# Optimization experiments

Measured on AMD Instinct MI355X. Metric: run time of the kernel, lower is better.

The kernel has to match this reference:

```python
import jax, jax.numpy as jnp
import numpy as np

N, R, M = 2048, 8, 4096  # samples, rank, signal length (M even)


def setup_inputs() -> dict:
    key = jax.random.key(0)
    kW, kH, kT = jax.random.split(key, 3)
    W = jax.random.normal(kW, (N, R), dtype=jnp.float32)
    H = jax.random.normal(kH, (R, M), dtype=jnp.float32)
    # tau are per-(sample, component) time shifts; modest positive values
    tau = jax.random.uniform(kT, (N, R), dtype=jnp.float32) * 5.0
    return {"W": W, "H": H, "tau": tau}


def reference(W, H, tau):
    # W: (N, R) raw weights, H: (R, M) raw sources, tau: (N, R) shifts
    M_ = H.shape[1]
    Nf = M_ // 2 + 1
    # one-sided spectrum of the (softplus-constrained) sources
    Hf = jnp.fft.fft(jax.nn.softplus(H), axis=1)[:, :Nf]            # (R, Nf) complex
    # rebuild full mirrored spectrum: [Hf, conj(flip(Hf[:, 1:Nf-1]))] -> (R, M)
    Hft = jnp.concatenate([Hf, jnp.conj(Hf[:, 1:Nf - 1][:, ::-1])], axis=1)
    f = jnp.arange(M_, dtype=H.dtype) / M_                          # (M,) normalized freqs
    # complex exponential shift operator, (N, R, M)
    omega = jnp.exp(-2j * jnp.pi * jnp.einsum('nd,m->ndm', tau, f))
    Wf = jax.nn.softplus(W)[:, :, None] * omega                     # (N, R, M)
    # reduce over rank: V[n, m] = sum_d Wf[n, d, m] * Hft[d, m]
    V = jnp.einsum('ndm,dm->nm', Wf, Hft)                           # (N, M) complex
    return V
```

## Files before the change

kernel.cpp:

```cpp
#include <hip/hip_runtime.h>
#include <math.h>

#define MLEN 4096
#define RANK 8
#define NSAMP 2048
#define VEC 4
#define NS  4

__device__ __forceinline__ float softplus_f(float x) {
    return (x > 20.0f) ? x : log1pf(expf(x));
}

__global__ __launch_bounds__(1024) void fft_rows_kernel(const float* __restrict__ H,
                                                        float2* __restrict__ Hft) {
    __shared__ float2 buf[MLEN];
    const int d = blockIdx.x;
    const float* row = H + d * MLEN;

    for (int i = threadIdx.x; i < MLEN; i += 1024) {
        unsigned x = __brev((unsigned)i) >> 20;
        unsigned src = ((x & 0x555u) << 1) | ((x & 0xAAAu) >> 1);
        buf[i] = make_float2(softplus_f(row[src]), 0.0f);
    }
    __syncthreads();

    for (int s = 0; s < 6; ++s) {
        const int quarter = 1 << (2 * s);
        const int p  = threadIdx.x;
        const int k  = p & (quarter - 1);
        const int j  = p >> (2 * s);
        const int i0 = (j << (2 * s + 2)) + k;
        const int i1 = i0 + quarter;
        const int i2 = i1 + quarter;
        const int i3 = i2 + quarter;
        const float ang = -6.28318530717958647692f * (float)k / (float)(quarter << 2);
        const float c1 = __cosf(ang), s1 = __sinf(ang);
        const float c2 = c1 * c1 - s1 * s1, s2 = 2.0f * c1 * s1;
        const float c3 = c1 * c2 - s1 * s2, s3 = c1 * s2 + s1 * c2;

        float2 a = buf[i0];
        float2 b = buf[i1];
        float2 c = buf[i2];
        float2 e = buf[i3];
        b = make_float2(b.x * c1 - b.y * s1, b.x * s1 + b.y * c1);
        c = make_float2(c.x * c2 - c.y * s2, c.x * s2 + c.y * c2);
        e = make_float2(e.x * c3 - e.y * s3, e.x * s3 + e.y * c3);

        const float2 t0 = make_float2(a.x + c.x, a.y + c.y);
        const float2 t1 = make_float2(a.x - c.x, a.y - c.y);
        const float2 t2 = make_float2(b.x + e.x, b.y + e.y);
        const float2 t3 = make_float2(b.y - e.y, e.x - b.x);

        buf[i0] = make_float2(t0.x + t2.x, t0.y + t2.y);
        buf[i1] = make_float2(t1.x + t3.x, t1.y + t3.y);
        buf[i2] = make_float2(t0.x - t2.x, t0.y - t2.y);
        buf[i3] = make_float2(t1.x - t3.x, t1.y - t3.y);
        __syncthreads();
    }

    float2* outrow = Hft + d * MLEN;
    for (int i = threadIdx.x; i < MLEN; i += 1024) outrow[i] = buf[i];
}

template <int REAL_ONLY>
__global__ __launch_bounds__(256) void mix_kernel(const float* __restrict__ W,
                                                  const float* __restrict__ tau,
                                                  const float2* __restrict__ Hft,
                                                  float* __restrict__ out) {
    const int tid = threadIdx.x;
    const int m0  = blockIdx.x * (256 * VEC) + tid;
    const int n0  = blockIdx.y * NS;

    __shared__ float  s_spw[NS * RANK];
    __shared__ float  s_tau[NS * RANK];
    __shared__ float2 s_step[NS * RANK];
    if (tid < NS * RANK) {
        const float t = tau[n0 * RANK + tid];
        s_spw[tid] = softplus_f(W[n0 * RANK + tid]);
        s_tau[tid] = t;
        const float a1 = -0.39269908169872415481f * t;
        s_step[tid] = make_float2(__cosf(a1), __sinf(a1));
    }
    __syncthreads();

    float ar[NS][VEC];
    float ai[NS][VEC];
#pragma unroll
    for (int j = 0; j < NS; ++j)
#pragma unroll
        for (int k = 0; k < VEC; ++k) { ar[j][k] = 0.0f; ai[j][k] = 0.0f; }

    const float th0f = -6.28318530717958647692f * ((float)m0 * (1.0f / (float)MLEN));

#pragma unroll 1
    for (int d = 0; d < RANK; ++d) {
        float cs[NS], sn[NS], dc[NS], ds[NS];
#pragma unroll
        for (int j = 0; j < NS; ++j) {
            const float t   = s_tau[j * RANK + d];
            const float spw = s_spw[j * RANK + d];
            const float a0  = th0f * t;
            cs[j] = spw * __cosf(a0);
            sn[j] = spw * __sinf(a0);
            const float2 st = s_step[j * RANK + d];
            dc[j] = st.x;
            ds[j] = st.y;
        }
        const float2* __restrict__ hrow = Hft + d * MLEN + m0;
        float2 hv[VEC];
#pragma unroll
        for (int k = 0; k < VEC; ++k) hv[k] = hrow[k * 256];
#pragma unroll
        for (int k = 0; k < VEC; ++k) {
#pragma unroll
            for (int j = 0; j < NS; ++j) {
                ar[j][k] += cs[j] * hv[k].x - sn[j] * hv[k].y;
                if (!REAL_ONLY) ai[j][k] += cs[j] * hv[k].y + sn[j] * hv[k].x;
                if (k < VEC - 1) {
                    const float ncs = cs[j] * dc[j] - sn[j] * ds[j];
                    sn[j] = cs[j] * ds[j] + sn[j] * dc[j];
                    cs[j] = ncs;
                }
            }
        }
    }

#pragma unroll
    for (int j = 0; j < NS; ++j) {
#pragma unroll
        for (int k = 0; k < VEC; ++k) {
            const size_t idx = (size_t)(n0 + j) * MLEN + m0 + k * 256;
            if (REAL_ONLY) out[idx] = ar[j][k];
            else ((float2*)out)[idx] = make_float2(ar[j][k], ai[j][k]);
        }
    }
}

extern "C" void kernel_launch(void* const* d_in, const int* in_sizes, int n_in,
                              void* d_out, int out_size, void* d_ws, size_t ws_size,
                              hipStream_t stream) {
    const float* W   = (const float*)d_in[0];
    const float* H   = (const float*)d_in[1];
    const float* tau = (const float*)d_in[2];
    float2* Hft = (float2*)d_ws;
    float* out  = (float*)d_out;

    fft_rows_kernel<<<RANK, 1024, 0, stream>>>(H, Hft);

    const long long NM = (long long)NSAMP * MLEN;
    dim3 grid(MLEN / (256 * VEC), NSAMP / NS);
    if ((long long)out_size >= 2 * NM) {
        mix_kernel<0><<<grid, 256, 0, stream>>>(W, tau, Hft, out);
    } else {
        mix_kernel<1><<<grid, 256, 0, stream>>>(W, tau, Hft, out);
    }
}
```

Measured before the change: 37.15 us.

## Split FFT into two wave-shuffle passes and vectorize mix kernel with contiguous columns

The single 8-block radix-4 shared-memory FFT is replaced by a four-step 64x64 FFT that uses wavefront shuffles across two kernels with 128 blocks each. This spreads the FFT over many more CUs, at the cost of an extra launch and a global intermediate buffer. The mix kernel now gives each thread 8 contiguous columns, loads Hft with float4, double-buffers the next rank's loads, and writes output with float4 stores. The longer twiddle recurrence chain (7 steps) may accumulate more float error.

```diff
diff --git a/kernel.cpp b/kernel.cpp
--- a/kernel.cpp
+++ b/kernel.cpp
@@ -4,62 +4,93 @@
 #define MLEN 4096
 #define RANK 8
 #define NSAMP 2048
-#define VEC 4
+#define VEC 8
 #define NS  4
 
 __device__ __forceinline__ float softplus_f(float x) {
     return (x > 20.0f) ? x : log1pf(expf(x));
 }
 
-__global__ __launch_bounds__(1024) void fft_rows_kernel(const float* __restrict__ H,
-                                                        float2* __restrict__ Hft) {
-    __shared__ float2 buf[MLEN];
-    const int d = blockIdx.x;
-    const float* row = H + d * MLEN;
+__device__ __forceinline__ float2 cmulf(float2 a, float2 b) {
+    return make_float2(a.x * b.x - a.y * b.y, a.x * b.y + a.y * b.x);
+}
 
-    for (int i = threadIdx.x; i < MLEN; i += 1024) {
-        unsigned x = __brev((unsigned)i) >> 20;
-        unsigned src = ((x & 0x555u) << 1) | ((x & 0xAAAu) >> 1);
-        buf[i] = make_float2(softplus_f(row[src]), 0.0f);
+__device__ __forceinline__ float2 wave_fft64(float2 v, int l) {
+#pragma unroll
+    for (int h = 32; h >= 1; h >>= 1) {
+        const float tx = __shfl_xor(v.x, h);
+        const float ty = __shfl_xor(v.y, h);
+        const bool hi = (l & h) != 0;
+        const float s = hi ? -1.0f : 1.0f;
+        float2 u = make_float2(fmaf(s, v.x, tx), fmaf(s, v.y, ty));
+        const int idx = hi ? (l & (h - 1)) : 0;
+        const float ang = -3.14159265358979323846f * (float)idx / (float)h;
+        const float cw = __cosf(ang), sw = __sinf(ang);
+        v = make_float2(u.x * cw - u.y * sw, u.x * sw + u.y * cw);
     }
-    __syncthreads();
+    return v;
+}
 
-    for (int s = 0; s < 6; ++s) {
-        const int quarter = 1 << (2 * s);
-        const int p  = threadIdx.x;
-        const int k  = p & (quarter - 1);
-        const int j  = p >> (2 * s);
-        const int i0 = (j << (2 * s + 2)) + k;
-        const int i1 = i0 + quarter;
-        const int i2 = i1 + quarter;
-        const int i3 = i2 + quarter;
-        const float ang = -6.28318530717958647692f * (float)k / (float)(quarter << 2);
-        const float c1 = __cosf(ang), s1 = __sinf(ang);
-        const float c2 = c1 * c1 - s1 * s1, s2 = 2.0f * c1 * s1;
-        const float c3 = c1 * c2 - s1 * s2, s3 = c1 * s2 + s1 * c2;
+__global__ __launch_bounds__(256) void fftA_kernel(const float* __restrict__ H,
+                                                   float2* __restrict__ Z) {
+    const int wid = (blockIdx.x << 2) + (threadIdx.x >> 6);
+    const int l   = threadIdx.x & 63;
+    const int d   = wid >> 6;
+    const int n2  = wid & 63;
 
-        float2 a = buf[i0];
-        float2 b = buf[i1];
-        float2 c = buf[i2];
-        float2 e = buf[i3];
-        b = make_float2(b.x * c1 - b.y * s1, b.x * s1 + b.y * c1);
-        c = make_float2(c.x * c2 - c.y * s2, c.x * s2 + c.y * c2);
-        e = make_float2(e.x * c3 - e.y * s3, e.x * s3 + e.y * c3);
+    const float x = softplus_f(H[d * MLEN + (l << 6) + n2]);
+    float2 v = wave_fft64(make_float2(x, 0.0f), l);
+    const int k1 = (int)(__brev((unsigned)l) >> 26);
+    const float ang = -3.14159265358979323846f / 2048.0f * (float)(n2 * k1);
+    v = cmulf(v, make_float2(__cosf(ang), __sinf(ang)));
+    Z[d * MLEN + (k1 << 6) + n2] = v;
+}
 
-        const float2 t0 = make_float2(a.x + c.x, a.y + c.y);
-        const float2 t1 = make_float2(a.x - c.x, a.y - c.y);
-        const float2 t2 = make_float2(b.x + e.x, b.y + e.y);
-        const float2 t3 = make_float2(b.y - e.y, e.x - b.x);
+__global__ __launch_bounds__(256) void fftB_kernel(const float2* __restrict__ Z,
+                                                   float2* __restrict__ Hft) {
+    const int wid = (blockIdx.x << 2) + (threadIdx.x >> 6);
+    const int l   = threadIdx.x & 63;
+    const int d   = wid >> 6;
+    const int k1  = wid & 63;
 
-        buf[i0] = make_float2(t0.x + t2.x, t0.y + t2.y);
-        buf[i1] = make_float2(t1.x + t3.x, t1.y + t3.y);
-        buf[i2] = make_float2(t0.x - t2.x, t0.y - t2.y);
-        buf[i3] = make_float2(t1.x - t3.x, t1.y - t3.y);
-        __syncthreads();
+    float2 v = Z[d * MLEN + (k1 << 6) + l];
+    v = wave_fft64(v, l);
+    const int k2 = (int)(__brev((unsigned)l) >> 26);
+    Hft[d * MLEN + (k2 << 6) + k1] = v;
+}
+
+template <int REAL_ONLY>
+__device__ __forceinline__ void accum_rank(int d,
+    const float4& h0, const float4& h1, const float4& h2, const float4& h3,
+    const float* s_spw, const float* s_tau, const float2* s_step,
+    float thm, float (&ar)[NS][VEC], float (&ai)[NS][VEC]) {
+    float cs[NS], sn[NS], dc[NS], ds[NS];
+#pragma unroll
+    for (int j = 0; j < NS; ++j) {
+        const float t   = s_tau[j * RANK + d];
+        const float spw = s_spw[j * RANK + d];
+        const float a0  = thm * t;
+        cs[j] = spw * __cosf(a0);
+        sn[j] = spw * __sinf(a0);
+        const float2 st = s_step[j * RANK + d];
+        dc[j] = st.x; ds[j] = st.y;
     }
-
-    float2* outrow = Hft + d * MLEN;
-    for (int i = threadIdx.x; i < MLEN; i += 1024) outrow[i] = buf[i];
+#pragma unroll
+    for (int k = 0; k < VEC; ++k) {
+        const float4& hq = (k < 2) ? h0 : (k < 4) ? h1 : (k < 6) ? h2 : h3;
+        const float hx = (k & 1) ? hq.z : hq.x;
+        const float hy = (k & 1) ? hq.w : hq.y;
+#pragma unroll
+        for (int j = 0; j < NS; ++j) {
+            ar[j][k] += cs[j] * hx - sn[j] * hy;
+            if (!REAL_ONLY) ai[j][k] += cs[j] * hy + sn[j] * hx;
+            if (k < VEC - 1) {
+                const float ncs = cs[j] * dc[j] - sn[j] * ds[j];
+                sn[j] = cs[j] * ds[j] + sn[j] * dc[j];
+                cs[j] = ncs;
+            }
+        }
+    }
 }
 
 template <int REAL_ONLY>
@@ -68,7 +99,7 @@
                                                   const float2* __restrict__ Hft,
                                                   float* __restrict__ out) {
     const int tid = threadIdx.x;
-    const int m0  = blockIdx.x * (256 * VEC) + tid;
+    const int m0  = (blockIdx.x * 256 + tid) * VEC;
     const int n0  = blockIdx.y * NS;
 
     __shared__ float  s_spw[NS * RANK];
@@ -78,7 +109,7 @@
         const float t = tau[n0 * RANK + tid];
         s_spw[tid] = softplus_f(W[n0 * RANK + tid]);
         s_tau[tid] = t;
-        const float a1 = -0.39269908169872415481f * t;
+        const float a1 = -1.53398078788564122971e-3f * t;
         s_step[tid] = make_float2(__cosf(a1), __sinf(a1));
     }
     __syncthreads();
@@ -90,48 +121,39 @@
 #pragma unroll
         for (int k = 0; k < VEC; ++k) { ar[j][k] = 0.0f; ai[j][k] = 0.0f; }
 
-    const float th0f = -6.28318530717958647692f * ((float)m0 * (1.0f / (float)MLEN));
+    const float thm = -6.28318530717958647692f * ((float)m0 * (1.0f / (float)MLEN));
+
+    const float4* p0 = reinterpret_cast<const float4*>(Hft + m0);
+    float4 hA0 = p0[0], hA1 = p0[1], hA2 = p0[2], hA3 = p0[3];
 
 #pragma unroll 1
-    for (int d = 0; d < RANK; ++d) {
-        float cs[NS], sn[NS], dc[NS], ds[NS];
-#pragma unroll
-        for (int j = 0; j < NS; ++j) {
-            const float t   = s_tau[j * RANK + d];
-            const float spw = s_spw[j * RANK + d];
-            const float a0  = th0f * t;
-            cs[j] = spw * __cosf(a0);
-            sn[j] = spw * __sinf(a0);
-            const float2 st = s_step[j * RANK + d];
-            dc[j] = st.x;
-            ds[j] = st.y;
+    for (int d = 0; d < RANK; d += 2) {
+        const float4* pB = reinterpret_cast<const float4*>(Hft + (d + 1) * MLEN + m0);
+        float4 hB0 = pB[0], hB1 = pB[1], hB2 = pB[2], hB3 = pB[3];
+        accum_rank<REAL_ONLY>(d, hA0, hA1, hA2, hA3, s_spw, s_tau, s_step, thm, ar, ai);
+        if (d + 2 < RANK) {
+            const float4* pA = reinterpret_cast<const float4*>(Hft + (d + 2) * MLEN + m0);
+            hA0 = pA[0]; hA1 = pA[1]; hA2 = pA[2]; hA3 = pA[3];
         }
-        const float2* __restrict__ hrow = Hft + d * MLEN + m0;
-        float2 hv[VEC];
-#pragma unroll
-        for (int k = 0; k < VEC; ++k) hv[k] = hrow[k * 256];
-#pragma unroll
-        for (int k = 0; k < VEC; ++k) {
-#pragma unroll
-            for (int j = 0; j < NS; ++j) {
-                ar[j][k] += cs[j] * hv[k].x - sn[j] * hv[k].y;
-                if (!REAL_ONLY) ai[j][k] += cs[j] * hv[k].y + sn[j] * hv[k].x;
-                if (k < VEC - 1) {
-                    const float ncs = cs[j] * dc[j] - sn[j] * ds[j];
-                    sn[j] = cs[j] * ds[j] + sn[j] * dc[j];
-                    cs[j] = ncs;
-                }
-            }
-        }
+        accum_rank<REAL_ONLY>(d + 1, hB0, hB1, hB2, hB3, s_spw, s_tau, s_step, thm, ar, ai);
     }
 
 #pragma unroll
     for (int j = 0; j < NS; ++j) {
+        if (REAL_ONLY) {
+            float* po = out + (size_t)(n0 + j) * MLEN + m0;
+            float4 o0 = make_float4(ar[j][0], ar[j][1], ar[j][2], ar[j][3]);
+            float4 o1 = make_float4(ar[j][4], ar[j][5], ar[j][6], ar[j][7]);
+            reinterpret_cast<float4*>(po)[0] = o0;
+            reinterpret_cast<float4*>(po)[1] = o1;
+        } else {
+            float2* po = (float2*)out + (size_t)(n0 + j) * MLEN + m0;
 #pragma unroll
-        for (int k = 0; k < VEC; ++k) {
-            const size_t idx = (size_t)(n0 + j) * MLEN + m0 + k * 256;
-            if (REAL_ONLY) out[idx] = ar[j][k];
-            else ((float2*)out)[idx] = make_float2(ar[j][k], ai[j][k]);
+            for (int q = 0; q < 4; ++q) {
+                float4 o = make_float4(ar[j][2 * q], ai[j][2 * q],
+                                       ar[j][2 * q + 1], ai[j][2 * q + 1]);
+                reinterpret_cast<float4*>(po)[q] = o;
+            }
         }
     }
 }
@@ -142,10 +164,12 @@
     const float* W   = (const float*)d_in[0];
     const float* H   = (const float*)d_in[1];
     const float* tau = (const float*)d_in[2];
-    float2* Hft = (float2*)d_ws;
+    float2* Z   = (float2*)d_ws;
+    float2* Hft = Z + RANK * MLEN;
     float* out  = (float*)d_out;
 
-    fft_rows_kernel<<<RANK, 1024, 0, stream>>>(H, Hft);
+    fftA_kernel<<<128, 256, 0, stream>>>(H, Z);
+    fftB_kernel<<<128, 256, 0, stream>>>(Z, Hft);
 
     const long long NM = (long long)NSAMP * MLEN;
     dim3 grid(MLEN / (256 * VEC), NSAMP / NS);
```

New measurement: 33.50 us. 9.8% less time.
